# Kernel tuning notes

Hardware: AMD Instinct MI355X
Metric: run time of the kernel (lower is better)

## Reference

```python
import jax, jax.numpy as jnp
import numpy as np

B = 4096
FLAT = 3 * 10 * 10 * 40  # 12000

def setup_inputs() -> dict:
    key = jax.random.key(0)
    ks = jax.random.split(key, 9)
    s = lambda fan_in: 1.0 / np.sqrt(fan_in)
    return {
        "x": jax.random.normal(ks[0], (B, 3, 10, 10, 40), dtype=jnp.float32),
        "conv_w": jax.random.normal(ks[1], (1, 3), dtype=jnp.float32) * s(3),   # Conv3d(3,1,k=1), no bias
        "F_w": jax.random.normal(ks[2], (3, 1), dtype=jnp.float32) * s(1),      # Conv3d(1,3,k=1), no bias
        "w1": jax.random.normal(ks[3], (4096, FLAT), dtype=jnp.float32) * s(FLAT),
        "b1": jnp.zeros((4096,), dtype=jnp.float32),
        "w2": jax.random.normal(ks[4], (512, 4096), dtype=jnp.float32) * s(4096),
        "b2": jnp.zeros((512,), dtype=jnp.float32),
        "w3": jax.random.normal(ks[5], (3, 512), dtype=jnp.float32) * s(512),
        "b3": jnp.zeros((3,), dtype=jnp.float32),
    }

def reference(x, conv_w, F_w, w1, b1, w2, b2, w3, b3):
    # Adaptive avg pools (input is exactly [B,3,10,10,40], so pools are plain means)
    xd = x.mean(axis=(3, 4), keepdims=True).transpose(0, 1, 4, 3, 2)  # [B,3,1,1,10]
    xh = x.mean(axis=(2, 4), keepdims=True).transpose(0, 1, 2, 4, 3)  # [B,3,1,1,10]
    xw = x.mean(axis=(2, 3), keepdims=True)                           # [B,3,1,1,40]
    cat = jnp.concatenate([xd, xh, xw], axis=4)                       # [B,3,1,1,60]
    y = jax.nn.relu(jnp.einsum('oc,bcdhw->bodhw', conv_w, cat))       # [B,1,1,1,60]
    sh = y[..., 10:20]  # [B,1,1,1,10]
    sw = y[..., 20:]    # [B,1,1,1,40]
    # NOTE: faithful to original code, which feeds x_h into the x_d branch.
    gd = jax.nn.sigmoid(jnp.einsum('oc,bcdhw->bodhw', F_w, sh.transpose(0, 1, 4, 3, 2)))  # [B,3,10,1,1]
    gh = jax.nn.sigmoid(jnp.einsum('oc,bcdhw->bodhw', F_w, sh.transpose(0, 1, 2, 4, 3)))  # [B,3,1,10,1]
    gw = jax.nn.sigmoid(jnp.einsum('oc,bcdhw->bodhw', F_w, sw))                            # [B,3,1,1,40]
    z = x * gd * gh * gw                      # [B,3,10,10,40]
    z = z.reshape(z.shape[0], -1)             # [B,12000]
    z = jax.nn.relu(z @ w1.T + b1)
    z = jax.nn.relu(z @ w2.T + b2)
    z = z @ w3.T + b3                          # [B,3]
    norm = jnp.linalg.norm(z, axis=1, keepdims=True)
    return z / jnp.maximum(norm, 1e-12)
```

## Files before the change

### kernel.cpp

```cpp
#include <hip/hip_runtime.h>
#include <hip/hip_fp16.h>

typedef _Float16 f16_t;
typedef __attribute__((ext_vector_type(8))) _Float16 f16x8;
typedef __attribute__((ext_vector_type(4))) _Float16 f16x4;
typedef __attribute__((ext_vector_type(4))) float f32x4;

__device__ __forceinline__ void gload_lds16(const void* g, void* lds) {
    __builtin_amdgcn_global_load_lds(
        (const __attribute__((address_space(1))) unsigned int*)g,
        (__attribute__((address_space(3))) unsigned int*)lds,
        16, 0, 0);
}

__device__ __forceinline__ float sigmoidf_(float v) {
    return 1.0f / (1.0f + expf(-v));
}

__global__ __launch_bounds__(256) void gate_kernel(
    const float* __restrict__ x, const float* __restrict__ conv_w,
    const float* __restrict__ F_w, f16_t* __restrict__ G) {
    __shared__ alignas(16) float xs[12000];
    __shared__ float part[240];
    __shared__ float mW[120];
    __shared__ float sv[10];
    __shared__ float tv[40];
    __shared__ float gsv[3][10];
    __shared__ float gwv[3][40];

    const int t = threadIdx.x;
    const long b = blockIdx.x;
    const float4* xp = (const float4*)(x + b * 12000);
    float4* xs4 = (float4*)xs;
    for (int i = t; i < 3000; i += 256) xs4[i] = xp[i];
    __syncthreads();

    if (t < 240) {
        int c = t / 80, h = (t % 80) / 8, g = t % 8;
        const float* p = xs + c * 4000 + h * 40 + g * 5;
        float s = 0.f;
        #pragma unroll
        for (int d = 0; d < 10; ++d)
            #pragma unroll
            for (int j = 0; j < 5; ++j) s += p[d * 400 + j];
        part[t] = s;
    }
    if (t < 120) {
        int c = t / 40, w = t % 40;
        const float* p = xs + c * 4000 + w;
        float s = 0.f;
        #pragma unroll
        for (int d = 0; d < 10; ++d)
            #pragma unroll
            for (int h = 0; h < 10; ++h) s += p[d * 400 + h * 40];
        mW[t] = s;
    }
    __syncthreads();
    if (t < 10) {
        float a = 0.f;
        #pragma unroll
        for (int c = 0; c < 3; ++c) {
            float m = 0.f;
            #pragma unroll
            for (int g = 0; g < 8; ++g) m += part[c * 80 + t * 8 + g];
            a += conv_w[c] * (m * (1.f / 400.f));
        }
        sv[t] = fmaxf(a, 0.f);
    }
    if (t < 40) {
        float a = 0.f;
        #pragma unroll
        for (int c = 0; c < 3; ++c) a += conv_w[c] * (mW[c * 40 + t] * (1.f / 100.f));
        tv[t] = fmaxf(a, 0.f);
    }
    __syncthreads();
    if (t < 30) { int c = t / 10, k = t % 10; gsv[c][k] = sigmoidf_(F_w[c] * sv[k]); }
    if (t < 120) { int c = t / 40, w = t % 40; gwv[c][w] = sigmoidf_(F_w[c] * tv[w]); }
    __syncthreads();

    f16x4* Gp = (f16x4*)(G + b * 12032);
    for (int i = t; i < 3000; i += 256) {
        int flat = i * 4;
        int c = flat / 4000, rem = flat % 4000;
        int d = rem / 400, rem2 = rem % 400;
        int h = rem2 / 40, w0 = rem2 % 40;
        float gdh = gsv[c][d] * gsv[c][h];
        float4 v = xs4[i];
        f16x4 o;
        o[0] = (f16_t)(v.x * gdh * gwv[c][w0 + 0]);
        o[1] = (f16_t)(v.y * gdh * gwv[c][w0 + 1]);
        o[2] = (f16_t)(v.z * gdh * gwv[c][w0 + 2]);
        o[3] = (f16_t)(v.w * gdh * gwv[c][w0 + 3]);
        Gp[i] = o;
    }
    if (t < 8) Gp[3000 + t] = (f16x4){};
}

__global__ __launch_bounds__(256) void cvt_f16_pad(
    const float* __restrict__ in, f16_t* __restrict__ out) {
    const long r = blockIdx.x;
    const float4* ip = (const float4*)(in + r * 12000);
    f16x4* op = (f16x4*)(out + r * 12032);
    for (int i = threadIdx.x; i < 3000; i += 256) {
        float4 v = ip[i];
        f16x4 o;
        o[0] = (f16_t)v.x; o[1] = (f16_t)v.y; o[2] = (f16_t)v.z; o[3] = (f16_t)v.w;
        op[i] = o;
    }
    if (threadIdx.x < 8) op[3000 + threadIdx.x] = (f16x4){};
}

__global__ __launch_bounds__(256) void cvt_f16(
    const float* __restrict__ in, f16_t* __restrict__ out, long n4) {
    long stride = (long)gridDim.x * 256;
    for (long i = (long)blockIdx.x * 256 + threadIdx.x; i < n4; i += stride) {
        float4 v = ((const float4*)in)[i];
        f16x4 o;
        o[0] = (f16_t)v.x; o[1] = (f16_t)v.y; o[2] = (f16_t)v.z; o[3] = (f16_t)v.w;
        ((f16x4*)out)[i] = o;
    }
}

__global__ __launch_bounds__(512) void gemm1_8phase(
    const f16_t* __restrict__ A, const f16_t* __restrict__ B,
    const float* __restrict__ bias, f16_t* __restrict__ C,
    int M, int N, int K2, int NT) {
    __shared__ alignas(16) f16_t lds[65536];
    const int t = threadIdx.x;
    const int lane = t & 63, w = t >> 6;
    const int wr = w >> 2, wc = w & 3;
    const int l15 = lane & 15, lg = lane >> 4;
    const long tileM = (long)blockIdx.y * 256;
    const long tileN = (long)blockIdx.x * 256;
    const long lK2 = K2;

    const int CH0 = (w * 2 + 0) * 64 + lane;
    const int CH1 = (w * 2 + 1) * 64 + lane;
    const int pr0 = CH0 >> 3, cc0 = (CH0 & 7) ^ (pr0 & 7);
    const int pr1 = CH1 >> 3, cc1 = (CH1 & 7) ^ (pr1 & 7);

    auto stageA = [&](int dst, long kk) {
        f16_t* db = lds + dst * 32768;
        gload_lds16(A + (tileM + pr0) * lK2 + kk + cc0 * 8, db + CH0 * 8);
        gload_lds16(A + (tileM + pr1) * lK2 + kk + cc1 * 8, db + CH1 * 8);
        gload_lds16(A + (tileM + 128 + pr0) * lK2 + kk + cc0 * 8, db + 8192 + CH0 * 8);
        gload_lds16(A + (tileM + 128 + pr1) * lK2 + kk + cc1 * 8, db + 8192 + CH1 * 8);
    };
    auto stageB = [&](int dst, long kk) {
        f16_t* db = lds + dst * 32768 + 16384;
        gload_lds16(B + (tileN + pr0) * lK2 + kk + cc0 * 8, db + CH0 * 8);
        gload_lds16(B + (tileN + pr1) * lK2 + kk + cc1 * 8, db + CH1 * 8);
        gload_lds16(B + (tileN + 128 + pr0) * lK2 + kk + cc0 * 8, db + 8192 + CH0 * 8);
        gload_lds16(B + (tileN + 128 + pr1) * lK2 + kk + cc1 * 8, db + 8192 + CH1 * 8);
    };

    const int sl = l15 & 7;
    const int aoff0 = wr * 8192 + l15 * 64 + (lg ^ sl) * 8;
    const int aoff1 = wr * 8192 + l15 * 64 + ((4 + lg) ^ sl) * 8;
    const int bbase = 16384 + (wc >> 1) * 8192 + (wc & 1) * 4096 + l15 * 64;
    const int boff0 = bbase + (lg ^ sl) * 8;
    const int boff1 = bbase + ((4 + lg) ^ sl) * 8;

    f32x4 acc[8][4] = {};

    stageA(0, 0);
    stageB(0, 0);
    if (NT > 1) { stageA(1, 64); stageB(1, 64); }

    for (int kt = 0; kt < NT; ++kt) {
        const int cur = kt & 1;
        const f16_t* bufc = lds + cur * 32768;
        if (kt + 1 < NT) asm volatile("s_waitcnt vmcnt(8)" ::: "memory");
        else             asm volatile("s_waitcnt vmcnt(0)" ::: "memory");
        __builtin_amdgcn_s_barrier();
        #pragma unroll
        for (int p = 0; p < 4; ++p) {
            const int qm = p >> 1, qn = p & 1;
            f16x8 af[4][2], bf[2][2];
            #pragma unroll
            for (int mf = 0; mf < 4; ++mf) {
                af[mf][0] = *(const f16x8*)(bufc + aoff0 + (qm * 64 + mf * 16) * 64);
                af[mf][1] = *(const f16x8*)(bufc + aoff1 + (qm * 64 + mf * 16) * 64);
            }
            #pragma unroll
            for (int nf = 0; nf < 2; ++nf) {
                bf[nf][0] = *(const f16x8*)(bufc + boff0 + (qn * 32 + nf * 16) * 64);
                bf[nf][1] = *(const f16x8*)(bufc + boff1 + (qn * 32 + nf * 16) * 64);
            }
            __builtin_amdgcn_s_barrier();
            asm volatile("s_waitcnt lgkmcnt(0)" ::: "memory");
            __builtin_amdgcn_s_setprio(1);
            #pragma unroll
            for (int mf = 0; mf < 4; ++mf)
                #pragma unroll
                for (int nf = 0; nf < 2; ++nf) {
                    acc[qm * 4 + mf][qn * 2 + nf] = __builtin_amdgcn_mfma_f32_16x16x32_f16(
                        af[mf][0], bf[nf][0], acc[qm * 4 + mf][qn * 2 + nf], 0, 0, 0);
                    acc[qm * 4 + mf][qn * 2 + nf] = __builtin_amdgcn_mfma_f32_16x16x32_f16(
                        af[mf][1], bf[nf][1], acc[qm * 4 + mf][qn * 2 + nf], 0, 0, 0);
                }
            __builtin_amdgcn_s_setprio(0);
            __builtin_amdgcn_s_barrier();
        }
        if (kt + 2 < NT) {
            const long kkn = (long)(kt + 2) * 64;
            stageA(cur, kkn);
            stageB(cur, kkn);
        }
    }

    const long rowC0 = tileM + wr * 128 + lg * 4;
    const long colC0 = tileN + wc * 64 + l15;
    #pragma unroll
    for (int ni = 0; ni < 4; ++ni) {
        long col = colC0 + ni * 16;
        float bia = bias[col];
        #pragma unroll
        for (int mi = 0; mi < 8; ++mi) {
            #pragma unroll
            for (int r = 0; r < 4; ++r) {
                long row = rowC0 + mi * 16 + r;
                float o = fmaxf(acc[mi][ni][r] + bia, 0.f);
                C[row * (long)N + col] = (f16_t)o;
            }
        }
    }
}

__global__ __launch_bounds__(256) void gemm2_nt(
    const f16_t* __restrict__ A, const f16_t* __restrict__ B,
    const float* __restrict__ bias, float* __restrict__ Cf,
    int M, int N, int K) {
    __shared__ alignas(16) f16_t As[64 * 32];
    __shared__ alignas(16) f16_t Bs[128 * 32];
    const int t = threadIdx.x;
    const int lane = t & 63, wid = t >> 6;
    const int wr = wid >> 1, wc = wid & 1;
    const int l15 = lane & 15, lg = lane >> 4;
    const long rowA0 = (long)blockIdx.y * 64;
    const long colB0 = (long)blockIdx.x * 128;

    const int eA = t * 8;
    const int rA = eA >> 5, kA = eA & 31;
    const int eB0 = t * 8;
    const int rB0 = eB0 >> 5, kB0 = eB0 & 31;
    const int eB1 = eB0 + 2048;
    const int rB1 = eB1 >> 5, kB1 = eB1 & 31;

    int aoff[2], boff[4];
    #pragma unroll
    for (int m = 0; m < 2; ++m) aoff[m] = (wr * 32 + m * 16 + l15) * 32 + lg * 8;
    #pragma unroll
    for (int n = 0; n < 4; ++n) boff[n] = (wc * 64 + n * 16 + l15) * 32 + lg * 8;

    f32x4 acc[2][4] = {};

    for (int kk = 0; kk < K; kk += 32) {
        __syncthreads();
        gload_lds16(A + (rowA0 + rA) * (long)K + kk + kA, As + eA);
        gload_lds16(B + (colB0 + rB0) * (long)K + kk + kB0, Bs + eB0);
        gload_lds16(B + (colB0 + rB1) * (long)K + kk + kB1, Bs + eB1);
        __syncthreads();

        f16x8 af[2], bfv[4];
        #pragma unroll
        for (int m = 0; m < 2; ++m) af[m] = *(const f16x8*)(As + aoff[m]);
        #pragma unroll
        for (int n = 0; n < 4; ++n) bfv[n] = *(const f16x8*)(Bs + boff[n]);
        #pragma unroll
        for (int m = 0; m < 2; ++m)
            #pragma unroll
            for (int n = 0; n < 4; ++n)
                acc[m][n] = __builtin_amdgcn_mfma_f32_16x16x32_f16(
                    af[m], bfv[n], acc[m][n], 0, 0, 0);
    }

    const long rowC0 = rowA0 + wr * 32 + lg * 4;
    const long colC0 = colB0 + wc * 64 + l15;
    #pragma unroll
    for (int n = 0; n < 4; ++n) {
        long col = colC0 + n * 16;
        float bia = bias[col];
        #pragma unroll
        for (int m = 0; m < 2; ++m) {
            #pragma unroll
            for (int r = 0; r < 4; ++r) {
                long row = rowC0 + m * 16 + r;
                float o = fmaxf(acc[m][n][r] + bia, 0.f);
                Cf[row * (long)N + col] = o;
            }
        }
    }
}

__global__ __launch_bounds__(256) void head_kernel(
    const float* __restrict__ z2, const float* __restrict__ w3,
    const float* __restrict__ b3, float* __restrict__ out) {
    const int lane = threadIdx.x & 63, wid = threadIdx.x >> 6;
    const long b = (long)blockIdx.x * 4 + wid;
    const float4* zp = (const float4*)(z2 + b * 512);
    float4 z0 = zp[lane * 2], z1 = zp[lane * 2 + 1];
    float d[3];
    #pragma unroll
    for (int o = 0; o < 3; ++o) {
        const float4* wp = (const float4*)(w3 + o * 512);
        float4 a0 = wp[lane * 2], a1 = wp[lane * 2 + 1];
        d[o] = z0.x * a0.x + z0.y * a0.y + z0.z * a0.z + z0.w * a0.w +
               z1.x * a1.x + z1.y * a1.y + z1.z * a1.z + z1.w * a1.w;
    }
    #pragma unroll
    for (int o = 0; o < 3; ++o)
        #pragma unroll
        for (int off = 1; off < 64; off <<= 1) d[o] += __shfl_xor(d[o], off);
    float d0 = d[0] + b3[0], d1 = d[1] + b3[1], d2 = d[2] + b3[2];
    float nrm = fmaxf(sqrtf(d0 * d0 + d1 * d1 + d2 * d2), 1e-12f);
    if (lane < 3) {
        float v = (lane == 0) ? d0 : (lane == 1) ? d1 : d2;
        out[b * 3 + lane] = v / nrm;
    }
}

extern "C" void kernel_launch(void* const* d_in, const int* in_sizes, int n_in,
                              void* d_out, int out_size, void* d_ws, size_t ws_size,
                              hipStream_t stream) {
    const float* x      = (const float*)d_in[0];
    const float* conv_w = (const float*)d_in[1];
    const float* F_w    = (const float*)d_in[2];
    const float* w1     = (const float*)d_in[3];
    const float* b1     = (const float*)d_in[4];
    const float* w2     = (const float*)d_in[5];
    const float* b2     = (const float*)d_in[6];
    const float* w3     = (const float*)d_in[7];
    const float* b3     = (const float*)d_in[8];
    float* out = (float*)d_out;

    char* ws = (char*)d_ws;
    f16_t* G   = (f16_t*)(ws);
    f16_t* w1h = (f16_t*)(ws + 98566144L);
    f16_t* z1  = (f16_t*)(ws + 197132288L);
    f16_t* w2h = (f16_t*)(ws + 230686720L);
    float* z2  = (float*)(ws);

    gate_kernel<<<4096, 256, 0, stream>>>(x, conv_w, F_w, G);
    cvt_f16_pad<<<4096, 256, 0, stream>>>(w1, w1h);
    cvt_f16<<<512, 256, 0, stream>>>(w2, w2h, 524288L);
    gemm1_8phase<<<dim3(16, 16), 512, 0, stream>>>(G, w1h, b1, z1, 4096, 4096, 12032, 188);
    gemm2_nt<<<dim3(4, 64), 256, 0, stream>>>(z1, w2h, b2, z2, 4096, 512, 4096);
    head_kernel<<<1024, 256, 0, stream>>>(z2, w3, b3, out);
}
```

Baseline: 652.1 us.

## Restructure GEMM1 main loop into K-half phases with interleaved prefetch

Reworks the large GEMM1 main loop so each 64-wide K tile is processed as two 32-wide halves. Each half is laid out in LDS with a new XOR swizzle, and the next tile's matching half is prefetched right after the current fragments are read. The aim is finer-grained overlap of global-to-LDS loads with MFMA work and fewer wasted waits. It also adds a launch_bounds occupancy hint of 2 and reorders the MFMA loop. The hint may constrain registers against the 128-float accumulator array, and with 128KB of LDS per block a second block likely cannot be resident anyway.

Result: faster. 575.5 us (-11.7%).

```diff
diff --git a/kernel.cpp b/kernel.cpp
--- a/kernel.cpp
+++ b/kernel.cpp
@@ -121,7 +121,7 @@
     }
 }
 
-__global__ __launch_bounds__(512) void gemm1_8phase(
+__global__ __launch_bounds__(512, 2) void gemm1_kphase(
     const f16_t* __restrict__ A, const f16_t* __restrict__ B,
     const float* __restrict__ bias, f16_t* __restrict__ C,
     int M, int N, int K2, int NT) {
@@ -134,78 +134,66 @@
     const long tileN = (long)blockIdx.x * 256;
     const long lK2 = K2;
 
-    const int CH0 = (w * 2 + 0) * 64 + lane;
-    const int CH1 = (w * 2 + 1) * 64 + lane;
-    const int pr0 = CH0 >> 3, cc0 = (CH0 & 7) ^ (pr0 & 7);
-    const int pr1 = CH1 >> 3, cc1 = (CH1 & 7) ^ (pr1 & 7);
-
-    auto stageA = [&](int dst, long kk) {
-        f16_t* db = lds + dst * 32768;
-        gload_lds16(A + (tileM + pr0) * lK2 + kk + cc0 * 8, db + CH0 * 8);
-        gload_lds16(A + (tileM + pr1) * lK2 + kk + cc1 * 8, db + CH1 * 8);
-        gload_lds16(A + (tileM + 128 + pr0) * lK2 + kk + cc0 * 8, db + 8192 + CH0 * 8);
-        gload_lds16(A + (tileM + 128 + pr1) * lK2 + kk + cc1 * 8, db + 8192 + CH1 * 8);
+    const int srow = t >> 2;
+    const int gs8 = ((t & 3) ^ ((t >> 3) & 3)) * 8;
+    auto stage_half = [&](int dst, int ph, long kk) {
+        f16_t* dA = lds + dst * 32768 + ph * 8192;
+        f16_t* dB = dA + 16384;
+        gload_lds16(A + (tileM + srow) * lK2 + kk + gs8, dA + t * 8);
+        gload_lds16(A + (tileM + srow + 128) * lK2 + kk + gs8, dA + 4096 + t * 8);
+        gload_lds16(B + (tileN + srow) * lK2 + kk + gs8, dB + t * 8);
+        gload_lds16(B + (tileN + srow + 128) * lK2 + kk + gs8, dB + 4096 + t * 8);
     };
-    auto stageB = [&](int dst, long kk) {
-        f16_t* db = lds + dst * 32768 + 16384;
-        gload_lds16(B + (tileN + pr0) * lK2 + kk + cc0 * 8, db + CH0 * 8);
-        gload_lds16(B + (tileN + pr1) * lK2 + kk + cc1 * 8, db + CH1 * 8);
-        gload_lds16(B + (tileN + 128 + pr0) * lK2 + kk + cc0 * 8, db + 8192 + CH0 * 8);
-        gload_lds16(B + (tileN + 128 + pr1) * lK2 + kk + cc1 * 8, db + 8192 + CH1 * 8);
-    };
-
-    const int sl = l15 & 7;
-    const int aoff0 = wr * 8192 + l15 * 64 + (lg ^ sl) * 8;
-    const int aoff1 = wr * 8192 + l15 * 64 + ((4 + lg) ^ sl) * 8;
-    const int bbase = 16384 + (wc >> 1) * 8192 + (wc & 1) * 4096 + l15 * 64;
-    const int boff0 = bbase + (lg ^ sl) * 8;
-    const int boff1 = bbase + ((4 + lg) ^ sl) * 8;
+
+    const int sl8 = (lg ^ ((l15 >> 1) & 3)) * 8;
 
     f32x4 acc[8][4] = {};
 
-    stageA(0, 0);
-    stageB(0, 0);
-    if (NT > 1) { stageA(1, 64); stageB(1, 64); }
+    stage_half(0, 0, 0);
+    stage_half(0, 1, 32);
+    asm volatile("s_waitcnt vmcnt(4)" ::: "memory");
+    __builtin_amdgcn_s_barrier();
 
     for (int kt = 0; kt < NT; ++kt) {
-        const int cur = kt & 1;
-        const f16_t* bufc = lds + cur * 32768;
-        if (kt + 1 < NT) asm volatile("s_waitcnt vmcnt(8)" ::: "memory");
-        else             asm volatile("s_waitcnt vmcnt(0)" ::: "memory");
-        __builtin_amdgcn_s_barrier();
-        #pragma unroll
-        for (int p = 0; p < 4; ++p) {
-            const int qm = p >> 1, qn = p & 1;
-            f16x8 af[4][2], bf[2][2];
-            #pragma unroll
-            for (int mf = 0; mf < 4; ++mf) {
-                af[mf][0] = *(const f16x8*)(bufc + aoff0 + (qm * 64 + mf * 16) * 64);
-                af[mf][1] = *(const f16x8*)(bufc + aoff1 + (qm * 64 + mf * 16) * 64);
-            }
-            #pragma unroll
-            for (int nf = 0; nf < 2; ++nf) {
-                bf[nf][0] = *(const f16x8*)(bufc + boff0 + (qn * 32 + nf * 16) * 64);
-                bf[nf][1] = *(const f16x8*)(bufc + boff1 + (qn * 32 + nf * 16) * 64);
-            }
+        const int c = kt & 1;
+        const f16_t* bufc = lds + c * 32768;
+        const bool more = (kt + 1 < NT);
+        #pragma unroll
+        for (int ph = 0; ph < 2; ++ph) {
+            f16x8 af[2][4], bf[2][2];
+            #pragma unroll
+            for (int qm = 0; qm < 2; ++qm)
+                #pragma unroll
+                for (int mf = 0; mf < 4; ++mf)
+                    af[qm][mf] = *(const f16x8*)(bufc + ph * 8192 +
+                        (wr * 128 + qm * 64 + mf * 16 + l15) * 32 + sl8);
+            #pragma unroll
+            for (int qn = 0; qn < 2; ++qn)
+                #pragma unroll
+                for (int nf = 0; nf < 2; ++nf)
+                    bf[qn][nf] = *(const f16x8*)(bufc + 16384 + ph * 8192 +
+                        (wc * 64 + qn * 32 + nf * 16 + l15) * 32 + sl8);
+            if (more) stage_half(c ^ 1, ph, (long)(kt + 1) * 64 + ph * 32);
             __builtin_amdgcn_s_barrier();
             asm volatile("s_waitcnt lgkmcnt(0)" ::: "memory");
+            __builtin_amdgcn_sched_barrier(0);
             __builtin_amdgcn_s_setprio(1);
             #pragma unroll
-            for (int mf = 0; mf < 4; ++mf)
+            for (int qn = 0; qn < 2; ++qn)
                 #pragma unroll
-                for (int nf = 0; nf < 2; ++nf) {
-                    acc[qm * 4 + mf][qn * 2 + nf] = __builtin_amdgcn_mfma_f32_16x16x32_f16(
-                        af[mf][0], bf[nf][0], acc[qm * 4 + mf][qn * 2 + nf], 0, 0, 0);
-                    acc[qm * 4 + mf][qn * 2 + nf] = __builtin_amdgcn_mfma_f32_16x16x32_f16(
-                        af[mf][1], bf[nf][1], acc[qm * 4 + mf][qn * 2 + nf], 0, 0, 0);
-                }
+                for (int nf = 0; nf < 2; ++nf)
+                    #pragma unroll
+                    for (int qm = 0; qm < 2; ++qm)
+                        #pragma unroll
+                        for (int mf = 0; mf < 4; ++mf)
+                            acc[qm * 4 + mf][qn * 2 + nf] =
+                                __builtin_amdgcn_mfma_f32_16x16x32_f16(
+                                    af[qm][mf], bf[qn][nf],
+                                    acc[qm * 4 + mf][qn * 2 + nf], 0, 0, 0);
             __builtin_amdgcn_s_setprio(0);
+            if (more) asm volatile("s_waitcnt vmcnt(4)" ::: "memory");
+            else      asm volatile("s_waitcnt vmcnt(0)" ::: "memory");
             __builtin_amdgcn_s_barrier();
-        }
-        if (kt + 2 < NT) {
-            const long kkn = (long)(kt + 2) * 64;
-            stageA(cur, kkn);
-            stageB(cur, kkn);
         }
     }
 
@@ -344,7 +332,7 @@
     gate_kernel<<<4096, 256, 0, stream>>>(x, conv_w, F_w, G);
     cvt_f16_pad<<<4096, 256, 0, stream>>>(w1, w1h);
     cvt_f16<<<512, 256, 0, stream>>>(w2, w2h, 524288L);
-    gemm1_8phase<<<dim3(16, 16), 512, 0, stream>>>(G, w1h, b1, z1, 4096, 4096, 12032, 188);
+    gemm1_kphase<<<dim3(16, 16), 512, 0, stream>>>(G, w1h, b1, z1, 4096, 4096, 12032, 188);
     gemm2_nt<<<dim3(4, 64), 256, 0, stream>>>(z1, w2h, b2, z2, 4096, 512, 4096);
     head_kernel<<<1024, 256, 0, stream>>>(z2, w3, b3, out);
 }
```
